# Performance work log

Hardware: AMD Instinct MI355X
Metric: run time of the kernel (lower is better)

Reference implementation:

```python
import jax, jax.numpy as jnp
import numpy as np

BETA = 0.9
TH = 1.0  # snn.Leaky default threshold
SPARSITY = 0.5


@jax.custom_vjp
def spike(x):
    # Heaviside spike; surrogate (atan, alpha=2) gradient as in snntorch default
    return (x > 0).astype(x.dtype)

def _spike_fwd(x):
    return spike(x), x

def _spike_bwd(x, g):
    return (g / (1.0 + (jnp.pi * x) ** 2),)

spike.defvjp(_spike_fwd, _spike_bwd)


def setup_inputs() -> dict:
    key = jax.random.key(0)
    ks = jax.random.split(key, 6)
    T, B, NIN, NH, NOUT = 50, 512, 784, 1000, 10

    def mk_w(k, o, i):
        k1, k2 = jax.random.split(k)
        w = jax.random.normal(k1, (o, i), jnp.float32) * (1.0 / np.sqrt(i))
        mask = (jax.random.uniform(k2, (o, i)) > SPARSITY).astype(jnp.float32)
        return w * mask

    x = jax.random.normal(ks[0], (T, B, NIN), jnp.float32)
    return dict(
        x=x,
        W0=mk_w(ks[1], NH, NIN), b0=jnp.zeros((NH,), jnp.float32),
        W1=mk_w(ks[2], NH, NH), b1=jnp.zeros((NH,), jnp.float32),
        W2=mk_w(ks[3], NH, NH), b2=jnp.zeros((NH,), jnp.float32),
        W3=mk_w(ks[4], NOUT, NH), b3=jnp.zeros((NOUT,), jnp.float32),
    )


def reference(x, W0, b0, W1, b1, W2, b2, W3, b3):
    params = ((W0, b0), (W1, b1), (W2, b2), (W3, b3))
    B = x.shape[1]
    mems0 = tuple(jnp.zeros((B, W.shape[0]), x.dtype) for W, _ in params)

    def step(mems, xt):
        inp = xt
        new_mems, spks = [], []
        for (W, b), m in zip(params, mems):
            cur = inp @ W.T + b
            # snntorch Leaky (reset_mechanism='subtract'):
            # reset from previous mem (detached), then mem = beta*mem + I - reset*th
            reset = jax.lax.stop_gradient((m > TH).astype(x.dtype))
            m_new = BETA * m + cur - reset * TH
            s = spike(m_new - TH)
            new_mems.append(m_new)
            spks.append(s)
            inp = s
        return tuple(new_mems), (tuple(spks), tuple(new_mems))

    _, (spk_rec, mem_rec) = jax.lax.scan(step, mems0, x)
    # spk_rec/mem_rec: tuples of [T, B, dim] arrays per layer
    return (*spk_rec, *mem_rec)
```

## Files before the change

kernel.cpp:

```cpp
#include <hip/hip_runtime.h>


typedef int int4v  __attribute__((ext_vector_type(4)));
typedef int int16v __attribute__((ext_vector_type(16)));

#define XSCALE 68719476736.0
#define WSCALE 1099511627776.0
#define TC 10

__global__ void wsplit_i8(const float* __restrict__ W, signed char* __restrict__ out,
                          int Nreal, int Npad, int K, int Kpad)
{
    int idx = blockIdx.x * blockDim.x + threadIdx.x;
    int total = Npad * Kpad;
    if (idx >= total) return;
    int n = idx / Kpad, k = idx - n * Kpad;
    long long v = 0;
    if (n < Nreal && k < K) v = __double2ll_rn((double)W[(size_t)n * K + k] * WSCALE);
    size_t plane = (size_t)total;
#pragma unroll
    for (int p = 0; p < 4; ++p) {
        int d = (int)(v & 255); if (d > 127) d -= 256;
        out[p * plane + idx] = (signed char)d;
        v = (v - d) >> 8;
    }
    out[4 * plane + idx] = (signed char)v;
}

__global__ void xsplit_chunk(const float* __restrict__ x, signed char* __restrict__ out)
{
    int idx = blockIdx.x * blockDim.x + threadIdx.x;
    if (idx >= 5120 * 832) return;
    int row = idx / 832, k = idx - row * 832;
    long long v = 0;
    if (k < 784) v = __double2ll_rn((double)x[(size_t)row * 784 + k] * XSCALE);
    const size_t plane = (size_t)5120 * 832;
    signed char* o = out + idx;
#pragma unroll
    for (int p = 0; p < 4; ++p) {
        int d = (int)(v & 255); if (d > 127) d -= 256;
        o[p * plane] = (signed char)d;
        v = (v - d) >> 8;
    }
    o[4 * plane] = (signed char)v;
}

template<int NA, int KP, int CS>
__global__ __launch_bounds__(256)
void gemm32(const signed char* __restrict__ Ap, size_t planeA,
            const signed char* __restrict__ Wp, size_t planeW,
            double* __restrict__ curout)
{
    __shared__ __align__(16) signed char Wld[5 * 64 * 80];
    __shared__ __align__(16) signed char Ald[NA * 64 * 80];
    constexpr int NIT = KP / 64;

    const int tid = threadIdx.x;
    const int l   = tid & 63;
    const int w   = tid >> 6;
    const int wm  = (w & 1) * 32;
    const int wn  = (w >> 1) * 32;
    const int r32 = l & 31;
    const int h   = l >> 5;

    const int bm = blockIdx.y * 64;
    const int bn = blockIdx.x * 64;

    const int srow = tid >> 2;
    const int sc   = (tid & 3) * 16;

    const signed char* ag = Ap + (size_t)(bm + srow) * KP + sc;
    const signed char* wg = Wp + (size_t)(bn + srow) * KP + sc;

    int4v Ar[NA], Wr[5];
#pragma unroll
    for (int p = 0; p < 5; ++p)  Wr[p] = *(const int4v*)(wg + p * planeW);
#pragma unroll
    for (int p = 0; p < NA; ++p) Ar[p] = *(const int4v*)(ag + p * planeA);

    int16v acc[5];
#pragma unroll
    for (int s = 0; s < 5; ++s)
#pragma unroll
        for (int r = 0; r < 16; ++r) acc[s][r] = 0;

    for (int it = 0; it < NIT; ++it) {
        __syncthreads();
#pragma unroll
        for (int p = 0; p < 5; ++p)
            *(int4v*)&Wld[(p * 64 + srow) * 80 + sc] = Wr[p];
#pragma unroll
        for (int p = 0; p < NA; ++p)
            *(int4v*)&Ald[(p * 64 + srow) * 80 + sc] = Ar[p];
        __syncthreads();

        if (it + 1 < NIT) {
            int kb = (it + 1) * 64;
#pragma unroll
            for (int p = 0; p < 5; ++p)
                Wr[p] = *(const int4v*)(wg + kb + p * planeW);
#pragma unroll
            for (int p = 0; p < NA; ++p)
                Ar[p] = *(const int4v*)(ag + kb + p * planeA);
        }

#pragma unroll
        for (int k2 = 0; k2 < 2; ++k2) {
            const int off = k2 * 32 + 16 * h;
            if constexpr (NA == 5) {
                int4v af[5], bq[5];
#pragma unroll
                for (int p = 0; p < 5; ++p)
                    af[p] = *(const int4v*)&Ald[(p * 64 + wm + r32) * 80 + off];
#pragma unroll
                for (int q = 0; q < 5; ++q)
                    bq[q] = *(const int4v*)&Wld[(q * 64 + wn + r32) * 80 + off];
#pragma unroll
                for (int q = 0; q < 5; ++q)
#pragma unroll
                    for (int p = 0; p < 5; ++p)
                        if (p + q >= 4)
                            acc[p + q - 4] = __builtin_amdgcn_mfma_i32_32x32x32_i8(
                                af[p], bq[q], acc[p + q - 4], 0, 0, 0);
            } else {
                int4v a0 = *(const int4v*)&Ald[(wm + r32) * 80 + off];
#pragma unroll
                for (int q = 0; q < 5; ++q) {
                    int4v bq = *(const int4v*)&Wld[(q * 64 + wn + r32) * 80 + off];
                    acc[q] = __builtin_amdgcn_mfma_i32_32x32x32_i8(a0, bq, acc[q], 0, 0, 0);
                }
            }
        }
    }

    const int col = bn + wn + r32;
    if (col < CS) {
#pragma unroll
        for (int reg = 0; reg < 16; ++reg) {
            int row = bm + wm + (reg & 3) + 8 * (reg >> 2) + 4 * h;
            double v = (double)acc[4][reg];
            v = v * 256.0 + (double)acc[3][reg];
            v = v * 256.0 + (double)acc[2][reg];
            v = v * 256.0 + (double)acc[1][reg];
            v = v * 256.0 + (double)acc[0][reg];
            curout[(size_t)row * CS + col] = v * (NA == 5 ? 0x1p-44 : 0x1p-40);
        }
    }
}

__global__ __launch_bounds__(256)
void if_update(const double* __restrict__ cur, const float* __restrict__ bias,
               double* __restrict__ mw, float* __restrict__ spk,
               float* __restrict__ mem, signed char* __restrict__ spk_i8,
               int N, int first)
{
    int idx = blockIdx.x * blockDim.x + threadIdx.x;
    if (idx >= 512 * N) return;
    int row = idx / N, col = idx - row * N;
    double mp = first ? 0.0 : mw[idx];
    double bs = (double)bias[col];
#pragma unroll 2
    for (int t = 0; t < TC; ++t) {
        double c   = cur[((size_t)t * 512 + row) * 1024 + col] + bs;
        double rst = (mp > 1.0) ? 1.0 : 0.0;
        double mn  = 0.9 * mp + c - rst;
        size_t o   = ((size_t)t * 512 + row) * N + col;
        spk[o] = (mn > 1.0) ? 1.0f : 0.0f;
        mem[o] = (float)mn;
        if (spk_i8)
            spk_i8[((size_t)t * 512 + row) * 1024 + col] = (signed char)((mn > 1.0) ? 1 : 0);
        mp = mn;
    }
    mw[idx] = mp;
}

__global__ __launch_bounds__(256)
void if3_kernel(const double* __restrict__ cur3, const float* __restrict__ bias,
                float* __restrict__ spk3, float* __restrict__ mem3)
{
    int idx = blockIdx.x * blockDim.x + threadIdx.x;
    if (idx >= 5120) return;
    int brow = idx / 10, col = idx - brow * 10;
    double bs = (double)bias[col];
    double mp = 0.0;
    for (int t = 0; t < 50; ++t) {
        double c   = cur3[((size_t)t * 512 + brow) * 16 + col] + bs;
        double rst = (mp > 1.0) ? 1.0 : 0.0;
        double mn  = 0.9 * mp + c - rst;
        size_t o   = (size_t)t * 5120 + (size_t)brow * 10 + col;
        spk3[o] = (mn > 1.0) ? 1.0f : 0.0f;
        mem3[o] = (float)mn;
        mp = mn;
    }
}

extern "C" void kernel_launch(void* const* d_in, const int* in_sizes, int n_in,
                              void* d_out, int out_size, void* d_ws, size_t ws_size,
                              hipStream_t stream)
{
    const float* x  = (const float*)d_in[0];
    const float* W0 = (const float*)d_in[1];
    const float* b0 = (const float*)d_in[2];
    const float* W1 = (const float*)d_in[3];
    const float* b1 = (const float*)d_in[4];
    const float* W2 = (const float*)d_in[5];
    const float* b2 = (const float*)d_in[6];
    const float* W3 = (const float*)d_in[7];
    const float* b3 = (const float*)d_in[8];
    float* out = (float*)d_out;

    const int T = 50;
    const size_t LNH = (size_t)512 * 1000;
    const size_t LNO = (size_t)512 * 10;

    float* spk0 = out;
    float* spk1 = spk0 + (size_t)T * LNH;
    float* spk2 = spk1 + (size_t)T * LNH;
    float* spk3 = spk2 + (size_t)T * LNH;
    float* mem0 = spk3 + (size_t)T * LNO;
    float* mem1 = mem0 + (size_t)T * LNH;
    float* mem2 = mem1 + (size_t)T * LNH;
    float* mem3 = mem2 + (size_t)T * LNH;

    double* cur = (double*)d_ws;
    double* mw0 = cur + (size_t)5120 * 1024;
    double* mw1 = mw0 + LNH;
    double* mw2 = mw1 + LNH;
    signed char* W0d = (signed char*)(mw2 + LNH);
    signed char* W1d = W0d + (size_t)5 * 1024 * 832;
    signed char* W2d = W1d + (size_t)5 * 1024 * 1024;
    signed char* W3d = W2d + (size_t)5 * 1024 * 1024;
    signed char* xsb = W3d + (size_t)5 * 64 * 1024;
    signed char* sp0 = xsb + (size_t)5 * 5120 * 832;
    signed char* sp1 = sp0 + (size_t)5120 * 1024;
    signed char* sp2 = sp1 + (size_t)5120 * 1024;

    hipMemsetAsync(sp0, 0, (size_t)2 * 5120 * 1024 + (size_t)25600 * 1024, stream);

    wsplit_i8<<<(1024 * 832  + 255) / 256, 256, 0, stream>>>(W0, W0d, 1000, 1024, 784,  832);
    wsplit_i8<<<(1024 * 1024 + 255) / 256, 256, 0, stream>>>(W1, W1d, 1000, 1024, 1000, 1024);
    wsplit_i8<<<(1024 * 1024 + 255) / 256, 256, 0, stream>>>(W2, W2d, 1000, 1024, 1000, 1024);
    wsplit_i8<<<(64 * 1024   + 255) / 256, 256, 0, stream>>>(W3, W3d, 10,   64,   1000, 1024);

    const size_t plA0 = (size_t)5120 * 832;
    const size_t plW0 = (size_t)1024 * 832;
    const size_t plWH = (size_t)1024 * 1024;
    const size_t plW3 = (size_t)64 * 1024;

    dim3 blk(256);
    dim3 gH(16, 80);
    dim3 g3(1, 400);

    for (int c = 0; c < T / TC; ++c) {
        const int t0 = c * TC;
        const int first = (c == 0);

        xsplit_chunk<<<(5120 * 832 + 255) / 256, 256, 0, stream>>>(
            x + (size_t)t0 * 512 * 784, xsb);

        gemm32<5, 832, 1024><<<gH, blk, 0, stream>>>(xsb, plA0, W0d, plW0, cur);
        if_update<<<2000, 256, 0, stream>>>(cur, b0, mw0,
            spk0 + (size_t)t0 * LNH, mem0 + (size_t)t0 * LNH, sp0, 1000, first);

        gemm32<1, 1024, 1024><<<gH, blk, 0, stream>>>(sp0, 0, W1d, plWH, cur);
        if_update<<<2000, 256, 0, stream>>>(cur, b1, mw1,
            spk1 + (size_t)t0 * LNH, mem1 + (size_t)t0 * LNH, sp1, 1000, first);

        gemm32<1, 1024, 1024><<<gH, blk, 0, stream>>>(sp1, 0, W2d, plWH, cur);
        if_update<<<2000, 256, 0, stream>>>(cur, b2, mw2,
            spk2 + (size_t)t0 * LNH, mem2 + (size_t)t0 * LNH,
            sp2 + (size_t)t0 * 512 * 1024, 1000, first);
    }

    gemm32<1, 1024, 16><<<g3, blk, 0, stream>>>(sp2, 0, W3d, plW3, cur);
    if3_kernel<<<20, 256, 0, stream>>>(cur, b3, spk3, mem3);
}
```

Measured before the change: 1.182 ms.

## Add 128-row tiled int8 GEMM for hidden layers and vectorize LIF update

Adds a specialized int8 MFMA GEMM for the spike-input hidden layers. It uses 128x64 block tiles with two M sub-tiles per warp, so each loaded weight fragment (5 byte planes) is reused across twice as many rows, and it register-prefetches the next K slice while computing the current one. The LIF update kernel now processes two columns per thread with double2/float2 loads and stores and a packed int8 spike store, cutting thread count and memory instructions. The trade-offs are higher register pressure from 10 accumulator tiles and half as many GEMM blocks.

```diff
diff --git a/kernel.cpp b/kernel.cpp
--- a/kernel.cpp
+++ b/kernel.cpp
@@ -148,30 +148,129 @@
     }
 }
 
+template<int KP>
+__global__ __launch_bounds__(256)
+void gemm32w(const signed char* __restrict__ Asp,
+             const signed char* __restrict__ Wp, size_t planeW,
+             double* __restrict__ curout)
+{
+    __shared__ __align__(16) signed char Wld[5 * 64 * 80];
+    __shared__ __align__(16) signed char Ald[128 * 80];
+    constexpr int NIT = KP / 64;
+
+    const int tid = threadIdx.x;
+    const int l   = tid & 63;
+    const int w   = tid >> 6;
+    const int wm  = (w & 1) * 64;
+    const int wn  = (w >> 1) * 32;
+    const int r32 = l & 31;
+    const int h   = l >> 5;
+
+    const int bm = blockIdx.y * 128;
+    const int bn = blockIdx.x * 64;
+
+    const int srA = tid >> 1;
+    const int scA = (tid & 1) * 32;
+    const int srW = tid >> 2;
+    const int scW = (tid & 3) * 16;
+
+    const signed char* ag = Asp + (size_t)(bm + srA) * KP + scA;
+    const signed char* wg = Wp  + (size_t)(bn + srW) * KP + scW;
+
+    int4v Ar0 = *(const int4v*)(ag);
+    int4v Ar1 = *(const int4v*)(ag + 16);
+    int4v Wr[5];
+#pragma unroll
+    for (int p = 0; p < 5; ++p) Wr[p] = *(const int4v*)(wg + p * planeW);
+
+    int16v acc[2][5];
+#pragma unroll
+    for (int mi = 0; mi < 2; ++mi)
+#pragma unroll
+        for (int s = 0; s < 5; ++s)
+#pragma unroll
+            for (int r = 0; r < 16; ++r) acc[mi][s][r] = 0;
+
+    for (int it = 0; it < NIT; ++it) {
+        __syncthreads();
+#pragma unroll
+        for (int p = 0; p < 5; ++p)
+            *(int4v*)&Wld[(p * 64 + srW) * 80 + scW] = Wr[p];
+        *(int4v*)&Ald[srA * 80 + scA]      = Ar0;
+        *(int4v*)&Ald[srA * 80 + scA + 16] = Ar1;
+        __syncthreads();
+
+        if (it + 1 < NIT) {
+            int kb = (it + 1) * 64;
+            Ar0 = *(const int4v*)(ag + kb);
+            Ar1 = *(const int4v*)(ag + kb + 16);
+#pragma unroll
+            for (int p = 0; p < 5; ++p)
+                Wr[p] = *(const int4v*)(wg + kb + p * planeW);
+        }
+
+#pragma unroll
+        for (int k2 = 0; k2 < 2; ++k2) {
+            const int off = k2 * 32 + 16 * h;
+            int4v bq[5];
+#pragma unroll
+            for (int q = 0; q < 5; ++q)
+                bq[q] = *(const int4v*)&Wld[(q * 64 + wn + r32) * 80 + off];
+#pragma unroll
+            for (int mi = 0; mi < 2; ++mi) {
+                int4v a0 = *(const int4v*)&Ald[(wm + mi * 32 + r32) * 80 + off];
+#pragma unroll
+                for (int q = 0; q < 5; ++q)
+                    acc[mi][q] = __builtin_amdgcn_mfma_i32_32x32x32_i8(
+                        a0, bq[q], acc[mi][q], 0, 0, 0);
+            }
+        }
+    }
+
+    const int col = bn + wn + r32;
+#pragma unroll
+    for (int mi = 0; mi < 2; ++mi)
+#pragma unroll
+        for (int reg = 0; reg < 16; ++reg) {
+            int row = bm + wm + mi * 32 + (reg & 3) + 8 * (reg >> 2) + 4 * h;
+            double v = (double)acc[mi][4][reg];
+            v = v * 256.0 + (double)acc[mi][3][reg];
+            v = v * 256.0 + (double)acc[mi][2][reg];
+            v = v * 256.0 + (double)acc[mi][1][reg];
+            v = v * 256.0 + (double)acc[mi][0][reg];
+            curout[(size_t)row * 1024 + col] = v * 0x1p-40;
+        }
+}
+
 __global__ __launch_bounds__(256)
 void if_update(const double* __restrict__ cur, const float* __restrict__ bias,
                double* __restrict__ mw, float* __restrict__ spk,
                float* __restrict__ mem, signed char* __restrict__ spk_i8,
-               int N, int first)
+               int first)
 {
     int idx = blockIdx.x * blockDim.x + threadIdx.x;
-    if (idx >= 512 * N) return;
-    int row = idx / N, col = idx - row * N;
-    double mp = first ? 0.0 : mw[idx];
-    double bs = (double)bias[col];
+    if (idx >= 512 * 500) return;
+    int row = idx / 500, col = (idx - row * 500) * 2;
+    double2 mp = first ? make_double2(0.0, 0.0)
+                       : *(const double2*)&mw[(size_t)row * 1000 + col];
+    double bs0 = (double)bias[col], bs1 = (double)bias[col + 1];
 #pragma unroll 2
     for (int t = 0; t < TC; ++t) {
-        double c   = cur[((size_t)t * 512 + row) * 1024 + col] + bs;
-        double rst = (mp > 1.0) ? 1.0 : 0.0;
-        double mn  = 0.9 * mp + c - rst;
-        size_t o   = ((size_t)t * 512 + row) * N + col;
-        spk[o] = (mn > 1.0) ? 1.0f : 0.0f;
-        mem[o] = (float)mn;
-        if (spk_i8)
-            spk_i8[((size_t)t * 512 + row) * 1024 + col] = (signed char)((mn > 1.0) ? 1 : 0);
-        mp = mn;
-    }
-    mw[idx] = mp;
+        double2 c = *(const double2*)&cur[((size_t)t * 512 + row) * 1024 + col];
+        double rst0 = (mp.x > 1.0) ? 1.0 : 0.0;
+        double rst1 = (mp.y > 1.0) ? 1.0 : 0.0;
+        double mn0 = 0.9 * mp.x + (c.x + bs0) - rst0;
+        double mn1 = 0.9 * mp.y + (c.y + bs1) - rst1;
+        int s0 = (mn0 > 1.0) ? 1 : 0;
+        int s1 = (mn1 > 1.0) ? 1 : 0;
+        size_t o = ((size_t)t * 512 + row) * 1000 + col;
+        *(float2*)&spk[o] = make_float2((float)s0, (float)s1);
+        *(float2*)&mem[o] = make_float2((float)mn0, (float)mn1);
+        *(short*)&spk_i8[((size_t)t * 512 + row) * 1024 + col] =
+            (short)(s0 | (s1 << 8));
+        mp.x = mn0; mp.y = mn1;
+    }
+    *(double2*)&mw[(size_t)row * 1000 + col] = mp;
 }
 
 __global__ __launch_bounds__(256)
@@ -248,7 +347,8 @@
     const size_t plW3 = (size_t)64 * 1024;
 
     dim3 blk(256);
-    dim3 gH(16, 80);
+    dim3 g0(16, 80);
+    dim3 gW(16, 40);
     dim3 g3(1, 400);
 
     for (int c = 0; c < T / TC; ++c) {
@@ -258,18 +358,18 @@
         xsplit_chunk<<<(5120 * 832 + 255) / 256, 256, 0, stream>>>(
             x + (size_t)t0 * 512 * 784, xsb);
 
-        gemm32<5, 832, 1024><<<gH, blk, 0, stream>>>(xsb, plA0, W0d, plW0, cur);
-        if_update<<<2000, 256, 0, stream>>>(cur, b0, mw0,
-            spk0 + (size_t)t0 * LNH, mem0 + (size_t)t0 * LNH, sp0, 1000, first);
-
-        gemm32<1, 1024, 1024><<<gH, blk, 0, stream>>>(sp0, 0, W1d, plWH, cur);
-        if_update<<<2000, 256, 0, stream>>>(cur, b1, mw1,
-            spk1 + (size_t)t0 * LNH, mem1 + (size_t)t0 * LNH, sp1, 1000, first);
-
-        gemm32<1, 1024, 1024><<<gH, blk, 0, stream>>>(sp1, 0, W2d, plWH, cur);
-        if_update<<<2000, 256, 0, stream>>>(cur, b2, mw2,
+        gemm32<5, 832, 1024><<<g0, blk, 0, stream>>>(xsb, plA0, W0d, plW0, cur);
+        if_update<<<1000, 256, 0, stream>>>(cur, b0, mw0,
+            spk0 + (size_t)t0 * LNH, mem0 + (size_t)t0 * LNH, sp0, first);
+
+        gemm32w<1024><<<gW, blk, 0, stream>>>(sp0, W1d, plWH, cur);
+        if_update<<<1000, 256, 0, stream>>>(cur, b1, mw1,
+            spk1 + (size_t)t0 * LNH, mem1 + (size_t)t0 * LNH, sp1, first);
+
+        gemm32w<1024><<<gW, blk, 0, stream>>>(sp1, W2d, plWH, cur);
+        if_update<<<1000, 256, 0, stream>>>(cur, b2, mw2,
             spk2 + (size_t)t0 * LNH, mem2 + (size_t)t0 * LNH,
-            sp2 + (size_t)t0 * 512 * 1024, 1000, first);
+            sp2 + (size_t)t0 * 512 * 1024, first);
     }
 
     gemm32<1, 1024, 16><<<g3, blk, 0, stream>>>(sp2, 0, W3d, plW3, cur);
```

Result: faster. 1.102 ms (-6.7%).

## Process all 50 timesteps per layer at once instead of chunks of ten

Applied to the files above, without the earlier changes.

Removes the 10-step chunk loop so each layer runs one large GEMM over all 25600 rows, followed by a single membrane-update kernel that walks all 50 timesteps with two columns per thread. This drops the carried-membrane workspace, the memset and the per-chunk x splitting, and merges the W1/W2 splits into one launch. The aim is fewer launches and larger, better-filled GEMM grids. In exchange the workspace for cur and the split x grows fivefold, and the update kernel loses parallelism across timesteps.

```diff
diff --git a/kernel.cpp b/kernel.cpp
--- a/kernel.cpp
+++ b/kernel.cpp
@@ -6,7 +6,7 @@
 
 #define XSCALE 68719476736.0
 #define WSCALE 1099511627776.0
-#define TC 10
+#define MT 25600
 
 __global__ void wsplit_i8(const float* __restrict__ W, signed char* __restrict__ out,
                           int Nreal, int Npad, int K, int Kpad)
@@ -27,14 +27,35 @@
     out[4 * plane + idx] = (signed char)v;
 }
 
-__global__ void xsplit_chunk(const float* __restrict__ x, signed char* __restrict__ out)
-{
-    int idx = blockIdx.x * blockDim.x + threadIdx.x;
-    if (idx >= 5120 * 832) return;
+__global__ void wsplit_i8x2(const float* __restrict__ Wa, signed char* __restrict__ oa,
+                            const float* __restrict__ Wb, signed char* __restrict__ ob)
+{
+    const float* W = blockIdx.y ? Wb : Wa;
+    signed char* out = blockIdx.y ? ob : oa;
+    int idx = blockIdx.x * blockDim.x + threadIdx.x;
+    const int total = 1024 * 1024;
+    if (idx >= total) return;
+    int n = idx >> 10, k = idx & 1023;
+    long long v = 0;
+    if (n < 1000 && k < 1000) v = __double2ll_rn((double)W[(size_t)n * 1000 + k] * WSCALE);
+    size_t plane = (size_t)total;
+#pragma unroll
+    for (int p = 0; p < 4; ++p) {
+        int d = (int)(v & 255); if (d > 127) d -= 256;
+        out[p * plane + idx] = (signed char)d;
+        v = (v - d) >> 8;
+    }
+    out[4 * plane + idx] = (signed char)v;
+}
+
+__global__ void xsplit_all(const float* __restrict__ x, signed char* __restrict__ out)
+{
+    int idx = blockIdx.x * blockDim.x + threadIdx.x;
+    if (idx >= MT * 832) return;
     int row = idx / 832, k = idx - row * 832;
     long long v = 0;
     if (k < 784) v = __double2ll_rn((double)x[(size_t)row * 784 + k] * XSCALE);
-    const size_t plane = (size_t)5120 * 832;
+    const size_t plane = (size_t)MT * 832;
     signed char* o = out + idx;
 #pragma unroll
     for (int p = 0; p < 4; ++p) {
@@ -143,35 +164,42 @@
             v = v * 256.0 + (double)acc[2][reg];
             v = v * 256.0 + (double)acc[1][reg];
             v = v * 256.0 + (double)acc[0][reg];
-            curout[(size_t)row * CS + col] = v * (NA == 5 ? 0x1p-44 : 0x1p-40);
+            curout[(size_t)row * (CS == 16 ? 16 : 1024) + col] =
+                v * (NA == 5 ? 0x1p-44 : 0x1p-40);
         }
     }
 }
 
 __global__ __launch_bounds__(256)
 void if_update(const double* __restrict__ cur, const float* __restrict__ bias,
-               double* __restrict__ mw, float* __restrict__ spk,
-               float* __restrict__ mem, signed char* __restrict__ spk_i8,
-               int N, int first)
-{
-    int idx = blockIdx.x * blockDim.x + threadIdx.x;
-    if (idx >= 512 * N) return;
-    int row = idx / N, col = idx - row * N;
-    double mp = first ? 0.0 : mw[idx];
-    double bs = (double)bias[col];
-#pragma unroll 2
-    for (int t = 0; t < TC; ++t) {
-        double c   = cur[((size_t)t * 512 + row) * 1024 + col] + bs;
-        double rst = (mp > 1.0) ? 1.0 : 0.0;
-        double mn  = 0.9 * mp + c - rst;
-        size_t o   = ((size_t)t * 512 + row) * N + col;
-        spk[o] = (mn > 1.0) ? 1.0f : 0.0f;
-        mem[o] = (float)mn;
-        if (spk_i8)
-            spk_i8[((size_t)t * 512 + row) * 1024 + col] = (signed char)((mn > 1.0) ? 1 : 0);
-        mp = mn;
-    }
-    mw[idx] = mp;
+               float* __restrict__ spk, float* __restrict__ mem,
+               signed char* __restrict__ spk_i8)
+{
+    int idx = blockIdx.x * blockDim.x + threadIdx.x;
+    if (idx >= 512 * 512) return;
+    int row = idx >> 9, col = (idx & 511) * 2;
+    if (col >= 1000) {
+        for (int t = 0; t < 50; ++t)
+            *(short*)&spk_i8[((size_t)t * 512 + row) * 1024 + col] = 0;
+        return;
+    }
+    double mp0 = 0.0, mp1 = 0.0;
+    double bs0 = (double)bias[col], bs1 = (double)bias[col + 1];
+    for (int t = 0; t < 50; ++t) {
+        double2 c = *(const double2*)&cur[((size_t)t * 512 + row) * 1024 + col];
+        double rst0 = (mp0 > 1.0) ? 1.0 : 0.0;
+        double rst1 = (mp1 > 1.0) ? 1.0 : 0.0;
+        double mn0 = 0.9 * mp0 + (c.x + bs0) - rst0;
+        double mn1 = 0.9 * mp1 + (c.y + bs1) - rst1;
+        int s0 = (mn0 > 1.0) ? 1 : 0;
+        int s1 = (mn1 > 1.0) ? 1 : 0;
+        size_t o = ((size_t)t * 512 + row) * 1000 + col;
+        *(float2*)&spk[o] = make_float2((float)s0, (float)s1);
+        *(float2*)&mem[o] = make_float2((float)mn0, (float)mn1);
+        *(short*)&spk_i8[((size_t)t * 512 + row) * 1024 + col] =
+            (short)(s0 | (s1 << 8));
+        mp0 = mn0; mp1 = mn1;
+    }
 }
 
 __global__ __launch_bounds__(256)
@@ -223,55 +251,36 @@
     float* mem3 = mem2 + (size_t)T * LNH;
 
     double* cur = (double*)d_ws;
-    double* mw0 = cur + (size_t)5120 * 1024;
-    double* mw1 = mw0 + LNH;
-    double* mw2 = mw1 + LNH;
-    signed char* W0d = (signed char*)(mw2 + LNH);
+    signed char* W0d = (signed char*)(cur + (size_t)MT * 1024);
     signed char* W1d = W0d + (size_t)5 * 1024 * 832;
     signed char* W2d = W1d + (size_t)5 * 1024 * 1024;
     signed char* W3d = W2d + (size_t)5 * 1024 * 1024;
     signed char* xsb = W3d + (size_t)5 * 64 * 1024;
-    signed char* sp0 = xsb + (size_t)5 * 5120 * 832;
-    signed char* sp1 = sp0 + (size_t)5120 * 1024;
-    signed char* sp2 = sp1 + (size_t)5120 * 1024;
-
-    hipMemsetAsync(sp0, 0, (size_t)2 * 5120 * 1024 + (size_t)25600 * 1024, stream);
-
-    wsplit_i8<<<(1024 * 832  + 255) / 256, 256, 0, stream>>>(W0, W0d, 1000, 1024, 784,  832);
-    wsplit_i8<<<(1024 * 1024 + 255) / 256, 256, 0, stream>>>(W1, W1d, 1000, 1024, 1000, 1024);
-    wsplit_i8<<<(1024 * 1024 + 255) / 256, 256, 0, stream>>>(W2, W2d, 1000, 1024, 1000, 1024);
-    wsplit_i8<<<(64 * 1024   + 255) / 256, 256, 0, stream>>>(W3, W3d, 10,   64,   1000, 1024);
-
-    const size_t plA0 = (size_t)5120 * 832;
+    signed char* sp0 = xsb + (size_t)5 * MT * 832;
+    signed char* sp1 = sp0 + (size_t)MT * 1024;
+    signed char* sp2 = sp1 + (size_t)MT * 1024;
+
+    wsplit_i8<<<(1024 * 832 + 255) / 256, 256, 0, stream>>>(W0, W0d, 1000, 1024, 784, 832);
+    wsplit_i8x2<<<dim3((1024 * 1024 + 255) / 256, 2), 256, 0, stream>>>(W1, W1d, W2, W2d);
+    wsplit_i8<<<(64 * 1024 + 255) / 256, 256, 0, stream>>>(W3, W3d, 10, 64, 1000, 1024);
+
+    xsplit_all<<<(MT * 832 + 255) / 256, 256, 0, stream>>>(x, xsb);
+
+    const size_t plA0 = (size_t)MT * 832;
     const size_t plW0 = (size_t)1024 * 832;
     const size_t plWH = (size_t)1024 * 1024;
     const size_t plW3 = (size_t)64 * 1024;
 
     dim3 blk(256);
-    dim3 gH(16, 80);
-    dim3 g3(1, 400);
-
-    for (int c = 0; c < T / TC; ++c) {
-        const int t0 = c * TC;
-        const int first = (c == 0);
-
-        xsplit_chunk<<<(5120 * 832 + 255) / 256, 256, 0, stream>>>(
-            x + (size_t)t0 * 512 * 784, xsb);
-
-        gemm32<5, 832, 1024><<<gH, blk, 0, stream>>>(xsb, plA0, W0d, plW0, cur);
-        if_update<<<2000, 256, 0, stream>>>(cur, b0, mw0,
-            spk0 + (size_t)t0 * LNH, mem0 + (size_t)t0 * LNH, sp0, 1000, first);
-
-        gemm32<1, 1024, 1024><<<gH, blk, 0, stream>>>(sp0, 0, W1d, plWH, cur);
-        if_update<<<2000, 256, 0, stream>>>(cur, b1, mw1,
-            spk1 + (size_t)t0 * LNH, mem1 + (size_t)t0 * LNH, sp1, 1000, first);
-
-        gemm32<1, 1024, 1024><<<gH, blk, 0, stream>>>(sp1, 0, W2d, plWH, cur);
-        if_update<<<2000, 256, 0, stream>>>(cur, b2, mw2,
-            spk2 + (size_t)t0 * LNH, mem2 + (size_t)t0 * LNH,
-            sp2 + (size_t)t0 * 512 * 1024, 1000, first);
-    }
-
+    dim3 gH(16, MT / 64);
+    dim3 g3(1, MT / 64);
+
+    gemm32<5, 832, 1024><<<gH, blk, 0, stream>>>(xsb, plA0, W0d, plW0, cur);
+    if_update<<<1024, 256, 0, stream>>>(cur, b0, spk0, mem0, sp0);
+    gemm32<1, 1024, 1024><<<gH, blk, 0, stream>>>(sp0, 0, W1d, plWH, cur);
+    if_update<<<1024, 256, 0, stream>>>(cur, b1, spk1, mem1, sp1);
+    gemm32<1, 1024, 1024><<<gH, blk, 0, stream>>>(sp1, 0, W2d, plWH, cur);
+    if_update<<<1024, 256, 0, stream>>>(cur, b2, spk2, mem2, sp2);
     gemm32<1, 1024, 16><<<g3, blk, 0, stream>>>(sp2, 0, W3d, plW3, cur);
     if3_kernel<<<20, 256, 0, stream>>>(cur, b3, spk3, mem3);
 }
```

Measured after the change: 1.168 ms. No clear change (-1.2%).
